# Performance work log

Hardware: AMD Instinct MI355X
Metric: run time of the kernel (lower is better)

Reference implementation:

```python
import jax, jax.numpy as jnp
import numpy as np

E, P, K, V, H, NE = 768, 256, 32, 32, 128, 8
B, M_DIM, T_DIM = 16, 4, 512


def setup_inputs() -> dict:
    key = jax.random.key(0)
    ks = jax.random.split(key, 24)
    s = 0.05
    inp = {
        'token_embeddings': jax.random.normal(ks[0], (B, M_DIM, T_DIM, E), jnp.float32),
        'U': jax.random.uniform(ks[1], (B, M_DIM, T_DIM), jnp.float32),
        'R': jax.random.uniform(ks[2], (B, M_DIM, M_DIM, T_DIM), jnp.float32),
        'S': jax.random.uniform(ks[3], (B, M_DIM, M_DIM, T_DIM), jnp.float32),
        'W_tp': jax.random.normal(ks[4], (E, P), jnp.float32) * s,
        'b_tp': jnp.zeros((P,), jnp.float32),
        'W_q': jax.random.normal(ks[5], (P, K), jnp.float32) * s,
        'b_q': jnp.zeros((K,), jnp.float32),
        'W_k': jax.random.normal(ks[6], (2, K), jnp.float32) * s,
        'b_k': jnp.zeros((K,), jnp.float32),
        'W_v': jax.random.normal(ks[7], (2, V), jnp.float32) * s,
        'b_v': jnp.zeros((V,), jnp.float32),
        'W_ih': jax.random.normal(ks[8], (3 * H, 1 + V), jnp.float32) * s,
        'W_hh': jax.random.normal(ks[9], (3 * H, H), jnp.float32) * s,
        'b_ih': jnp.zeros((3 * H,), jnp.float32),
        'b_hh': jnp.zeros((3 * H,), jnp.float32),
        'W1': jax.random.normal(ks[10], (P + H, (P + H) // 2), jnp.float32) * s,
        'b1': jnp.zeros(((P + H) // 2,), jnp.float32),
        'W2': jax.random.normal(ks[11], ((P + H) // 2, NE), jnp.float32) * s,
        'b2': jnp.zeros((NE,), jnp.float32),
        'M': M_DIM,
        'T': T_DIM,
    }
    return inp


def _gru(x, W_ih, W_hh, b_ih, b_hh):
    # x: [N, T, D] -> outputs [N, T, H]; PyTorch GRU cell math
    N, T, _ = x.shape
    Hh = W_hh.shape[1]
    gi = jnp.einsum('ntd,gd->ntg', x, W_ih) + b_ih  # [N,T,3H] precomputed input gates
    gi = jnp.transpose(gi, (1, 0, 2))  # [T,N,3H]

    def step(h, gi_t):
        gh = h @ W_hh.T + b_hh
        i_r, i_z, i_n = jnp.split(gi_t, 3, axis=-1)
        h_r, h_z, h_n = jnp.split(gh, 3, axis=-1)
        r = jax.nn.sigmoid(i_r + h_r)
        z = jax.nn.sigmoid(i_z + h_z)
        n = jnp.tanh(i_n + r * h_n)
        h_new = (1.0 - z) * n + z * h
        return h_new, h_new

    h0 = jnp.zeros((N, Hh), x.dtype)
    _, hs = jax.lax.scan(step, h0, gi)
    return jnp.transpose(hs, (1, 0, 2))  # [N,T,H]


def reference(token_embeddings, U, R, S, W_tp, b_tp, W_q, b_q, W_k, b_k, W_v, b_v,
              W_ih, W_hh, b_ih, b_hh, W1, b1, W2, b2, M, T):
    Bn, Mn, Tn, _ = token_embeddings.shape
    proc = jax.nn.relu(token_embeddings @ W_tp + b_tp)           # [B,M,T,P]
    query = proc @ W_q + b_q                                     # [B,M,T,K]
    Rp = jnp.transpose(R, (0, 3, 1, 2))                          # [B,T,M,M]
    Sp = jnp.transpose(S, (0, 3, 1, 2))
    pf = jnp.stack([Rp, Sp], axis=-1)                            # [B,T,M,M,2]
    keys = pf @ W_k + b_k                                        # [B,T,M,M,K]
    vals = pf @ W_v + b_v                                        # [B,T,M,M,V]
    scores = jnp.einsum('bmtk,btmjk->bmtj', query, keys) / np.sqrt(K)
    diag = jnp.eye(Mn, dtype=bool)                               # exclude j == m
    scores = jnp.where(diag[None, :, None, :], -1e9, scores)
    w = jax.nn.softmax(scores, axis=-1)                          # [B,M,T,M]
    ctx = jnp.einsum('bmtj,btmjv->bmtv', w, vals)                # [B,M,T,V]
    gru_in = jnp.concatenate([U[..., None], ctx], axis=-1)       # [B,M,T,1+V]
    gru_out = _gru(gru_in.reshape(Bn * Mn, Tn, 1 + V), W_ih, W_hh, b_ih, b_hh)
    rus_ctx = gru_out.reshape(Bn, Mn, Tn, H)
    combined = jnp.concatenate([proc, rus_ctx], axis=-1)         # [B,M,T,P+H]
    hidden = jax.nn.relu(combined @ W1 + b1)
    logits = hidden @ W2 + b2                                    # [B,M,T,NE]
    return logits
```

## Files before the change

kernel.cpp:

```cpp
#include <hip/hip_runtime.h>


typedef __attribute__((ext_vector_type(8))) short short8;
typedef __attribute__((ext_vector_type(4))) float f32x4;

__device__ __forceinline__ float bf2f(unsigned short u) {
    return __uint_as_float(((unsigned int)u) << 16);
}
__device__ __forceinline__ unsigned short f2bf(float f) {
    unsigned int x = __float_as_uint(f);
    return (unsigned short)((x + 0x7FFFu + ((x >> 16) & 1u)) >> 16);
}
__device__ __forceinline__ float sigm(float x) { return 1.0f / (1.0f + __expf(-x)); }
__device__ __forceinline__ float tanh_fast(float x) {
    x = fminf(fmaxf(x, -15.0f), 15.0f);
    float e = __expf(-2.0f * x);
    return (1.0f - e) / (1.0f + e);
}
__device__ __forceinline__ float dpp_xor1_add(float v) {
    int o = __builtin_amdgcn_update_dpp(0, __float_as_int(v), 0xB1, 0xF, 0xF, true);
    return v + __int_as_float(o);
}
__device__ __forceinline__ float sel4(f32x4 c, int sel) {
    float t0 = (sel & 1) ? c[1] : c[0];
    float t1 = (sel & 1) ? c[3] : c[2];
    return (sel & 2) ? t1 : t0;
}

#define CST_SC   768
#define CST_WU   800
#define CST_WA2  1184
#define CST_WB2  1568
#define CST_CC   1952

__global__ void k_paint(float* out, float val, int nmax) {
    int i = blockIdx.x * blockDim.x + threadIdx.x;
    if (i < nmax) out[i] = val;
}

__global__ void k_prep(const float* __restrict__ Wq,
                       const float* __restrict__ bq,
                       const float* __restrict__ Wk,
                       const float* __restrict__ bk,
                       const float* __restrict__ Wv,
                       const float* __restrict__ bv,
                       const float* __restrict__ Wih,
                       const float* __restrict__ bih,
                       float* __restrict__ cst)
{
    const int t = threadIdx.x;
    if (t < 256) {
        float a = 0.f, b = 0.f, c = 0.f;
        for (int k = 0; k < 32; ++k) {
            float w = Wq[t * 32 + k];
            a = fmaf(w, Wk[k], a);
            b = fmaf(w, Wk[32 + k], b);
            c = fmaf(w, bk[k], c);
        }
        cst[t] = a; cst[256 + t] = b; cst[512 + t] = c;
    }
    if (t == 0) {
        float ca = 0.f, cb = 0.f, cc = 0.f;
        for (int k = 0; k < 32; ++k) {
            float bqk = bq[k];
            ca = fmaf(bqk, Wk[k], ca);
            cb = fmaf(bqk, Wk[32 + k], cb);
            cc = fmaf(bqk, bk[k], cc);
        }
        cst[CST_SC + 0] = ca; cst[CST_SC + 1] = cb; cst[CST_SC + 2] = cc;
    }
    if (t < 384) {
        cst[CST_WU + t] = Wih[t * 33];
        float a2 = 0.f, b2 = 0.f, c2 = bih[t];
        for (int v = 0; v < 32; ++v) {
            float w = Wih[t * 33 + 1 + v];
            a2 = fmaf(w, Wv[v], a2);
            b2 = fmaf(w, Wv[32 + v], b2);
            c2 = fmaf(w, bv[v], c2);
        }
        cst[CST_WA2 + t] = a2; cst[CST_WB2 + t] = b2; cst[CST_CC + t] = c2;
    }
}

__global__ __launch_bounds__(256) void k_proc(
    const float* __restrict__ A,
    const float* __restrict__ Bw,
    const float* __restrict__ bias,
    unsigned short* __restrict__ C)
{
    __shared__ unsigned short A_s[64 * 40];
    __shared__ unsigned short B_s[64 * 40];
    const int t = threadIdx.x;
    const int row0 = blockIdx.y * 64;
    const int col0 = blockIdx.x * 64;
    const int lane = t & 63, wave = t >> 6;
    const int wr = wave >> 1, wc = wave & 1;
    const int quad = lane >> 4, l16 = lane & 15;

    f32x4 acc[2][2] = {};

    for (int k0 = 0; k0 < 768; k0 += 32) {
        {
            const int r = t >> 2, kq = (t & 3) * 8;
            const float* src = A + (size_t)(row0 + r) * 768 + k0 + kq;
            float4 v0 = *(const float4*)(src);
            float4 v1 = *(const float4*)(src + 4);
            short8 s;
            s[0] = f2bf(v0.x); s[1] = f2bf(v0.y); s[2] = f2bf(v0.z); s[3] = f2bf(v0.w);
            s[4] = f2bf(v1.x); s[5] = f2bf(v1.y); s[6] = f2bf(v1.z); s[7] = f2bf(v1.w);
            *(short8*)(A_s + r * 40 + kq) = s;
        }
        {
            const int k = t >> 3, nq = (t & 7) * 8;
            const float* src = Bw + (size_t)(k0 + k) * 256 + col0 + nq;
            float4 v0 = *(const float4*)(src);
            float4 v1 = *(const float4*)(src + 4);
            B_s[(nq + 0) * 40 + k] = f2bf(v0.x);
            B_s[(nq + 1) * 40 + k] = f2bf(v0.y);
            B_s[(nq + 2) * 40 + k] = f2bf(v0.z);
            B_s[(nq + 3) * 40 + k] = f2bf(v0.w);
            B_s[(nq + 4) * 40 + k] = f2bf(v1.x);
            B_s[(nq + 5) * 40 + k] = f2bf(v1.y);
            B_s[(nq + 6) * 40 + k] = f2bf(v1.z);
            B_s[(nq + 7) * 40 + k] = f2bf(v1.w);
        }
        __syncthreads();
        short8 af[2], bf[2];
        #pragma unroll
        for (int im = 0; im < 2; ++im)
            af[im] = *(const short8*)(A_s + (wr * 32 + im * 16 + l16) * 40 + quad * 8);
        #pragma unroll
        for (int in = 0; in < 2; ++in)
            bf[in] = *(const short8*)(B_s + (wc * 32 + in * 16 + l16) * 40 + quad * 8);
        #pragma unroll
        for (int im = 0; im < 2; ++im)
            #pragma unroll
            for (int in = 0; in < 2; ++in)
                acc[im][in] = __builtin_amdgcn_mfma_f32_16x16x32_bf16(
                    af[im], bf[in], acc[im][in], 0, 0, 0);
        __syncthreads();
    }
    float bias_v[2];
    #pragma unroll
    for (int in = 0; in < 2; ++in) bias_v[in] = bias[col0 + wc * 32 + in * 16 + l16];
    #pragma unroll
    for (int im = 0; im < 2; ++im)
        #pragma unroll
        for (int in = 0; in < 2; ++in) {
            const int c_g = col0 + wc * 32 + in * 16 + l16;
            #pragma unroll
            for (int reg = 0; reg < 4; ++reg) {
                const int r_g = row0 + wr * 32 + im * 16 + quad * 4 + reg;
                float v = fmaxf(acc[im][in][reg] + bias_v[in], 0.f);
                C[(size_t)r_g * 256 + c_g] = f2bf(v);
            }
        }
}

__global__ __launch_bounds__(256) void k_attn(
    const unsigned short* __restrict__ proc,
    const float* __restrict__ R,
    const float* __restrict__ S,
    const float* __restrict__ cst,
    float* __restrict__ wrws)
{
    __shared__ float wv_s[768];
    const int tid = threadIdx.x;
    for (int i = tid; i < 768; i += 256) wv_s[i] = cst[i];
    __syncthreads();

    const int lane = tid & 63, wave = tid >> 6;
    const int row = blockIdx.x * 4 + wave;
    const int t = row & 511, m = (row >> 9) & 3, b = row >> 11;
    const int p0 = lane * 4;

    ushort4 u = *(const ushort4*)(proc + (size_t)row * 256 + p0);
    float p0f = bf2f(u.x), p1f = bf2f(u.y), p2f = bf2f(u.z), p3f = bf2f(u.w);
    float dA = 0.f, dB = 0.f, dC = 0.f;
    dA = fmaf(p0f, wv_s[p0 + 0], dA); dB = fmaf(p0f, wv_s[256 + p0 + 0], dB); dC = fmaf(p0f, wv_s[512 + p0 + 0], dC);
    dA = fmaf(p1f, wv_s[p0 + 1], dA); dB = fmaf(p1f, wv_s[256 + p0 + 1], dB); dC = fmaf(p1f, wv_s[512 + p0 + 1], dC);
    dA = fmaf(p2f, wv_s[p0 + 2], dA); dB = fmaf(p2f, wv_s[256 + p0 + 2], dB); dC = fmaf(p2f, wv_s[512 + p0 + 2], dC);
    dA = fmaf(p3f, wv_s[p0 + 3], dA); dB = fmaf(p3f, wv_s[256 + p0 + 3], dB); dC = fmaf(p3f, wv_s[512 + p0 + 3], dC);
    #pragma unroll
    for (int mm = 1; mm < 64; mm <<= 1) {
        dA += __shfl_xor(dA, mm, 64);
        dB += __shfl_xor(dB, mm, 64);
        dC += __shfl_xor(dC, mm, 64);
    }
    if (lane == 0) {
        dA += cst[CST_SC + 0]; dB += cst[CST_SC + 1]; dC += cst[CST_SC + 2];
        const float scale = 0.17677669529663687f;
        float rr[4], ss[4], sc[4], mx = -1e30f;
        #pragma unroll
        for (int j = 0; j < 4; ++j) {
            const size_t idx = ((size_t)(b * 16 + m * 4 + j)) * 512 + t;
            rr[j] = R[idx]; ss[j] = S[idx];
            float v = (rr[j] * dA + ss[j] * dB + dC) * scale;
            if (j == m) v = -1e9f;
            sc[j] = v; mx = fmaxf(mx, v);
        }
        float w[4], se = 0.f;
        #pragma unroll
        for (int j = 0; j < 4; ++j) { w[j] = __expf(sc[j] - mx); se += w[j]; }
        const float inv = 1.0f / se;
        float wr = 0.f, wss = 0.f;
        #pragma unroll
        for (int j = 0; j < 4; ++j) { wr += w[j] * rr[j]; wss += w[j] * ss[j]; }
        float2 o; o.x = wr * inv; o.y = wss * inv;
        ((float2*)wrws)[row] = o;
    }
}

__global__ __launch_bounds__(256) void k_gru(
    const float* __restrict__ wrws,
    const float* __restrict__ U,
    const float* __restrict__ Whh,
    const float* __restrict__ bhh,
    const float* __restrict__ cst,
    unsigned short* __restrict__ gout)
{
    __shared__ unsigned short hbuf[2][2][144];
    __shared__ float4 uvw_s[512];

    const int tid  = threadIdx.x;
    const int lane = tid & 63, w = tid >> 6;
    const int l16  = lane & 15, quad = lane >> 4;
    const int n    = blockIdx.x;
    const int par  = l16 & 1;
    const int sel  = (l16 >> 1) & 3;
    const int hh   = (l16 >> 3) & 1;
    const int eg   = 32 * w + 16 * hh + quad * 4 + sel;
    const bool writer = (par == 0);

    short8 afr[3][2][4];
    #pragma unroll
    for (int g3 = 0; g3 < 3; ++g3)
        #pragma unroll
        for (int h2 = 0; h2 < 2; ++h2) {
            const int row = g3 * 128 + 32 * w + 16 * h2 + l16;
            const float* rp = Whh + (size_t)row * 128 + quad * 8;
            #pragma unroll
            for (int kf = 0; kf < 4; ++kf) {
                float4 v0 = *(const float4*)(rp + kf * 32);
                float4 v1 = *(const float4*)(rp + kf * 32 + 4);
                short8 s;
                s[0] = f2bf(v0.x); s[1] = f2bf(v0.y); s[2] = f2bf(v0.z); s[3] = f2bf(v0.w);
                s[4] = f2bf(v1.x); s[5] = f2bf(v1.y); s[6] = f2bf(v1.z); s[7] = f2bf(v1.w);
                afr[g3][h2][kf] = s;
            }
        }

    const float wu_r = cst[CST_WU  + eg], wu_z = cst[CST_WU  + 128 + eg], wu_n = cst[CST_WU  + 256 + eg];
    const float wa_r = cst[CST_WA2 + eg], wa_z = cst[CST_WA2 + 128 + eg], wa_n = cst[CST_WA2 + 256 + eg];
    const float wb_r = cst[CST_WB2 + eg], wb_z = cst[CST_WB2 + 128 + eg], wb_n = cst[CST_WB2 + 256 + eg];
    const float cc_r = cst[CST_CC  + eg] + bhh[eg];
    const float cc_z = cst[CST_CC  + 128 + eg] + bhh[128 + eg];
    const float cc_n = cst[CST_CC  + 256 + eg];
    const float bh_n = bhh[256 + eg];

    for (int i = tid; i < 512; i += 256) {
        float u = U[(size_t)n * 512 + i];
        float2 w2 = ((const float2*)wrws)[(size_t)n * 512 + i];
        float4 p; p.x = u; p.y = w2.x; p.z = w2.y; p.w = 0.f;
        uvw_s[i] = p;
    }
    for (int i = tid; i < 288; i += 256) ((unsigned int*)hbuf)[i] = 0u;
    __syncthreads();

    float h_old = 0.f;
    const f32x4 ZZ = {0.f, 0.f, 0.f, 0.f};

    #pragma unroll 2
    for (int t = 0; t < 512; ++t) {
        const int cur = t & 1, nxt = cur ^ 1;

        const unsigned short* hb = &hbuf[cur][par][0];
        short8 bfr[4];
        #pragma unroll
        for (int kf = 0; kf < 4; ++kf)
            bfr[kf] = *(const short8*)(hb + kf * 32 + quad * 8);
        const float4 uvw = uvw_s[t];

        f32x4 c[6] = {ZZ, ZZ, ZZ, ZZ, ZZ, ZZ};
        #pragma unroll
        for (int kf = 0; kf < 4; ++kf)
            #pragma unroll
            for (int j = 0; j < 6; ++j)
                c[j] = __builtin_amdgcn_mfma_f32_16x16x32_bf16(
                    afr[j >> 1][j & 1][kf], bfr[kf], c[j], 0, 0, 0);

        float gh[3];
        #pragma unroll
        for (int g3 = 0; g3 < 3; ++g3) {
            const float v0 = sel4(c[2 * g3 + 0], sel);
            const float v1 = sel4(c[2 * g3 + 1], sel);
            gh[g3] = dpp_xor1_add(hh ? v1 : v0);
        }

        const float gir = fmaf(uvw.z, wb_r, fmaf(uvw.y, wa_r, fmaf(uvw.x, wu_r, cc_r)));
        const float giz = fmaf(uvw.z, wb_z, fmaf(uvw.y, wa_z, fmaf(uvw.x, wu_z, cc_z)));
        const float gin = fmaf(uvw.z, wb_n, fmaf(uvw.y, wa_n, fmaf(uvw.x, wu_n, cc_n)));
        const float r  = sigm(gir + gh[0]);
        const float z  = sigm(giz + gh[1]);
        const float nn = tanh_fast(fmaf(r, gh[2] + bh_n, gin));
        const float hn = fmaf(z, h_old - nn, nn);
        h_old = hn;

        if (writer) {
            const unsigned short hi16 = f2bf(hn);
            hbuf[nxt][0][eg] = hi16;
            hbuf[nxt][1][eg] = f2bf(hn - bf2f(hi16));
            gout[((size_t)n * 512 + t) * 128 + eg] = hi16;
        }
        asm volatile("s_waitcnt lgkmcnt(0)" ::: "memory");
        __builtin_amdgcn_s_barrier();
        asm volatile("" ::: "memory");
        __builtin_amdgcn_sched_barrier(0x7);
    }
}

__global__ __launch_bounds__(256) void k_hid(
    const unsigned short* __restrict__ proc,
    const unsigned short* __restrict__ gout,
    const float* __restrict__ W1,
    const float* __restrict__ b1,
    const float* __restrict__ W2,
    const float* __restrict__ b2,
    float* __restrict__ out)
{
    __shared__ __align__(16) unsigned char smem[56352];
    unsigned short* As = (unsigned short*)smem;
    unsigned short* Bh = (unsigned short*)(smem + 5120);
    unsigned short* Bl = (unsigned short*)(smem + 20480);
    float* Hs  = (float*)smem;
    float* W2s = (float*)(smem + 50176);
    float* b2s = (float*)(smem + 56320);

    const int tid = threadIdx.x;
    const int row0 = blockIdx.x * 64;
    const int lane = tid & 63, w = tid >> 6;
    const int l16 = lane & 15, quad = lane >> 4;

    for (int i = tid; i < 1536; i += 256) W2s[i] = W2[i];
    if (tid < 8) b2s[tid] = b2[tid];

    const int ar = tid >> 2, akq = (tid & 3) * 8;
    const int bk2 = (tid >> 4) * 2, bc0 = tid & 15;

    f32x4 acc[4][3] = {};

    for (int k0 = 0; k0 < 384; k0 += 32) {
        __syncthreads();
        {
            const int kk = k0 + akq;
            short8 v;
            if (kk < 256) v = *(const short8*)(proc + (size_t)(row0 + ar) * 256 + kk);
            else          v = *(const short8*)(gout + (size_t)(row0 + ar) * 128 + (kk - 256));
            *(short8*)(As + ar * 40 + akq) = v;
        }
        {
            const float* wrow0 = W1 + (size_t)(k0 + bk2) * 192;
            const float* wrow1 = wrow0 + 192;
            #pragma unroll
            for (int j = 0; j < 12; ++j) {
                const int c = bc0 + 16 * j;
                const float f0 = wrow0[c], f1 = wrow1[c];
                const unsigned short h0 = f2bf(f0), h1 = f2bf(f1);
                const unsigned short s0 = f2bf(f0 - bf2f(h0));
                const unsigned short s1 = f2bf(f1 - bf2f(h1));
                *(unsigned int*)(Bh + c * 40 + bk2) = (unsigned int)h0 | ((unsigned int)h1 << 16);
                *(unsigned int*)(Bl + c * 40 + bk2) = (unsigned int)s0 | ((unsigned int)s1 << 16);
            }
        }
        __syncthreads();
        short8 af[4], bh[3], bl[3];
        #pragma unroll
        for (int m = 0; m < 4; ++m)
            af[m] = *(const short8*)(As + (m * 16 + l16) * 40 + quad * 8);
        #pragma unroll
        for (int nn = 0; nn < 3; ++nn) {
            const int col = w * 48 + nn * 16 + l16;
            bh[nn] = *(const short8*)(Bh + col * 40 + quad * 8);
            bl[nn] = *(const short8*)(Bl + col * 40 + quad * 8);
        }
        #pragma unroll
        for (int m = 0; m < 4; ++m)
            #pragma unroll
            for (int nn = 0; nn < 3; ++nn) {
                acc[m][nn] = __builtin_amdgcn_mfma_f32_16x16x32_bf16(af[m], bh[nn], acc[m][nn], 0, 0, 0);
                acc[m][nn] = __builtin_amdgcn_mfma_f32_16x16x32_bf16(af[m], bl[nn], acc[m][nn], 0, 0, 0);
            }
    }
    __syncthreads();
    {
        float b1v[3];
        #pragma unroll
        for (int nn = 0; nn < 3; ++nn) b1v[nn] = b1[w * 48 + nn * 16 + l16];
        #pragma unroll
        for (int m = 0; m < 4; ++m)
            #pragma unroll
            for (int nn = 0; nn < 3; ++nn) {
                const int col = w * 48 + nn * 16 + l16;
                #pragma unroll
                for (int reg = 0; reg < 4; ++reg) {
                    const int row = m * 16 + quad * 4 + reg;
                    Hs[row * 196 + col] = fmaxf(acc[m][nn][reg] + b1v[nn], 0.f);
                }
            }
    }
    __syncthreads();
    const int r = tid >> 2, qq = tid & 3;
    const int e0 = 2 * qq, e1 = 2 * qq + 1;
    float s0 = b2s[e0], s1 = b2s[e1];
    for (int c = 0; c < 192; ++c) {
        float h = Hs[r * 196 + c];
        s0 = fmaf(h, W2s[c * 8 + e0], s0);
        s1 = fmaf(h, W2s[c * 8 + e1], s1);
    }
    out[(size_t)(row0 + r) * 8 + e0] = s0;
    out[(size_t)(row0 + r) * 8 + e1] = s1;
}

extern "C" void kernel_launch(void* const* d_in, const int* in_sizes, int n_in,
                              void* d_out, int out_size, void* d_ws, size_t ws_size,
                              hipStream_t stream) {
    const float* emb  = (const float*)d_in[0];
    const float* U    = (const float*)d_in[1];
    const float* R    = (const float*)d_in[2];
    const float* S    = (const float*)d_in[3];
    const float* W_tp = (const float*)d_in[4];
    const float* b_tp = (const float*)d_in[5];
    const float* W_q  = (const float*)d_in[6];
    const float* b_q  = (const float*)d_in[7];
    const float* W_k  = (const float*)d_in[8];
    const float* b_k  = (const float*)d_in[9];
    const float* W_v  = (const float*)d_in[10];
    const float* b_v  = (const float*)d_in[11];
    const float* W_ih = (const float*)d_in[12];
    const float* W_hh = (const float*)d_in[13];
    const float* b_ih = (const float*)d_in[14];
    const float* b_hh = (const float*)d_in[15];
    const float* W1   = (const float*)d_in[16];
    const float* b1   = (const float*)d_in[17];
    const float* W2   = (const float*)d_in[18];
    const float* b2   = (const float*)d_in[19];

    float* outp = (float*)d_out;

    const size_t NEEDED = 25444352u;
    if (ws_size < NEEDED) {
        k_paint<<<(out_size + 255) / 256, 256, 0, stream>>>(outp, 3.0f, out_size);
        return;
    }

    char* ws = (char*)d_ws;
    unsigned short* proc = (unsigned short*)(ws);
    float*          wrws = (float*)(ws + 16777216u);
    unsigned short* gout = (unsigned short*)(ws + 17039360u);
    float*          cst  = (float*)(ws + 25427968u);

    k_prep<<<1, 512, 0, stream>>>(W_q, b_q, W_k, b_k, W_v, b_v, W_ih, b_ih, cst);
    k_proc<<<dim3(4, 512), 256, 0, stream>>>(emb, W_tp, b_tp, proc);
    k_attn<<<8192, 256, 0, stream>>>(proc, R, S, cst, wrws);
    k_gru <<<64, 256, 0, stream>>>(wrws, U, W_hh, b_hh, cst, gout);
    k_hid <<<512, 256, 0, stream>>>(proc, gout, W1, b1, W2, b2, outp);
}
```

Before: 530.6 us.

## Enlarge proc GEMM tile, defer GRU output stores, vectorize W2 dot

The projection GEMM now uses 128-row tiles, so each wave computes 4x2 MFMA tiles and the grid is halved. This gives more reuse of the B tile per load. In the GRU recurrence, both lane parities now write their own hbuf entry, removing the divergent writer branch. The global store of h is deferred by one step, and the next step's U/attention values are prefetched from LDS. The final hidden-to-logits dot product uses a transposed W2 in LDS and float4 reads to cut scalar LDS traffic.

```diff
diff --git a/kernel.cpp b/kernel.cpp
--- a/kernel.cpp
+++ b/kernel.cpp
@@ -88,27 +88,32 @@
     const float* __restrict__ bias,
     unsigned short* __restrict__ C)
 {
-    __shared__ unsigned short A_s[64 * 40];
+    __shared__ unsigned short A_s[128 * 40];
     __shared__ unsigned short B_s[64 * 40];
     const int t = threadIdx.x;
-    const int row0 = blockIdx.y * 64;
+    const int row0 = blockIdx.y * 128;
     const int col0 = blockIdx.x * 64;
     const int lane = t & 63, wave = t >> 6;
     const int wr = wave >> 1, wc = wave & 1;
     const int quad = lane >> 4, l16 = lane & 15;
 
-    f32x4 acc[2][2] = {};
+    f32x4 acc[4][2] = {};
 
     for (int k0 = 0; k0 < 768; k0 += 32) {
         {
-            const int r = t >> 2, kq = (t & 3) * 8;
+            const int r = t >> 1, kq = (t & 1) * 16;
             const float* src = A + (size_t)(row0 + r) * 768 + k0 + kq;
             float4 v0 = *(const float4*)(src);
             float4 v1 = *(const float4*)(src + 4);
-            short8 s;
-            s[0] = f2bf(v0.x); s[1] = f2bf(v0.y); s[2] = f2bf(v0.z); s[3] = f2bf(v0.w);
-            s[4] = f2bf(v1.x); s[5] = f2bf(v1.y); s[6] = f2bf(v1.z); s[7] = f2bf(v1.w);
-            *(short8*)(A_s + r * 40 + kq) = s;
+            float4 v2 = *(const float4*)(src + 8);
+            float4 v3 = *(const float4*)(src + 12);
+            short8 s0, s1;
+            s0[0] = f2bf(v0.x); s0[1] = f2bf(v0.y); s0[2] = f2bf(v0.z); s0[3] = f2bf(v0.w);
+            s0[4] = f2bf(v1.x); s0[5] = f2bf(v1.y); s0[6] = f2bf(v1.z); s0[7] = f2bf(v1.w);
+            s1[0] = f2bf(v2.x); s1[1] = f2bf(v2.y); s1[2] = f2bf(v2.z); s1[3] = f2bf(v2.w);
+            s1[4] = f2bf(v3.x); s1[5] = f2bf(v3.y); s1[6] = f2bf(v3.z); s1[7] = f2bf(v3.w);
+            *(short8*)(A_s + r * 40 + kq) = s0;
+            *(short8*)(A_s + r * 40 + kq + 8) = s1;
         }
         {
             const int k = t >> 3, nq = (t & 7) * 8;
@@ -125,15 +130,15 @@
             B_s[(nq + 7) * 40 + k] = f2bf(v1.w);
         }
         __syncthreads();
-        short8 af[2], bf[2];
-        #pragma unroll
-        for (int im = 0; im < 2; ++im)
-            af[im] = *(const short8*)(A_s + (wr * 32 + im * 16 + l16) * 40 + quad * 8);
+        short8 af[4], bf[2];
+        #pragma unroll
+        for (int im = 0; im < 4; ++im)
+            af[im] = *(const short8*)(A_s + (wr * 64 + im * 16 + l16) * 40 + quad * 8);
         #pragma unroll
         for (int in = 0; in < 2; ++in)
             bf[in] = *(const short8*)(B_s + (wc * 32 + in * 16 + l16) * 40 + quad * 8);
         #pragma unroll
-        for (int im = 0; im < 2; ++im)
+        for (int im = 0; im < 4; ++im)
             #pragma unroll
             for (int in = 0; in < 2; ++in)
                 acc[im][in] = __builtin_amdgcn_mfma_f32_16x16x32_bf16(
@@ -144,13 +149,13 @@
     #pragma unroll
     for (int in = 0; in < 2; ++in) bias_v[in] = bias[col0 + wc * 32 + in * 16 + l16];
     #pragma unroll
-    for (int im = 0; im < 2; ++im)
+    for (int im = 0; im < 4; ++im)
         #pragma unroll
         for (int in = 0; in < 2; ++in) {
             const int c_g = col0 + wc * 32 + in * 16 + l16;
             #pragma unroll
             for (int reg = 0; reg < 4; ++reg) {
-                const int r_g = row0 + wr * 32 + im * 16 + quad * 4 + reg;
+                const int r_g = row0 + wr * 64 + im * 16 + quad * 4 + reg;
                 float v = fmaxf(acc[im][in][reg] + bias_v[in], 0.f);
                 C[(size_t)r_g * 256 + c_g] = f2bf(v);
             }
@@ -230,7 +235,6 @@
     const int sel  = (l16 >> 1) & 3;
     const int hh   = (l16 >> 3) & 1;
     const int eg   = 32 * w + 16 * hh + quad * 4 + sel;
-    const bool writer = (par == 0);
 
     short8 afr[3][2][4];
     #pragma unroll
@@ -268,18 +272,22 @@
     __syncthreads();
 
     float h_old = 0.f;
+    unsigned short prev_hi = 0;
+    unsigned short* gp = gout + (size_t)n * 512 * 128 + eg;
+    float4 uvw = uvw_s[0];
     const f32x4 ZZ = {0.f, 0.f, 0.f, 0.f};
 
     #pragma unroll 2
     for (int t = 0; t < 512; ++t) {
         const int cur = t & 1, nxt = cur ^ 1;
 
+        if (t && par == 0) gp[(size_t)(t - 1) * 128] = prev_hi;
+
         const unsigned short* hb = &hbuf[cur][par][0];
         short8 bfr[4];
         #pragma unroll
         for (int kf = 0; kf < 4; ++kf)
             bfr[kf] = *(const short8*)(hb + kf * 32 + quad * 8);
-        const float4 uvw = uvw_s[t];
 
         f32x4 c[6] = {ZZ, ZZ, ZZ, ZZ, ZZ, ZZ};
         #pragma unroll
@@ -306,17 +314,20 @@
         const float hn = fmaf(z, h_old - nn, nn);
         h_old = hn;
 
-        if (writer) {
-            const unsigned short hi16 = f2bf(hn);
-            hbuf[nxt][0][eg] = hi16;
-            hbuf[nxt][1][eg] = f2bf(hn - bf2f(hi16));
-            gout[((size_t)n * 512 + t) * 128 + eg] = hi16;
-        }
+        const float4 uvw_n = uvw_s[(t + 1) & 511];
+
+        const unsigned short hi16 = f2bf(hn);
+        const unsigned short wv = par ? f2bf(hn - bf2f(hi16)) : hi16;
+        hbuf[nxt][par][eg] = wv;
+        prev_hi = hi16;
+
         asm volatile("s_waitcnt lgkmcnt(0)" ::: "memory");
         __builtin_amdgcn_s_barrier();
         asm volatile("" ::: "memory");
         __builtin_amdgcn_sched_barrier(0x7);
-    }
+        uvw = uvw_n;
+    }
+    if (par == 0) gp[(size_t)511 * 128] = prev_hi;
 }
 
 __global__ __launch_bounds__(256) void k_hid(
@@ -328,20 +339,23 @@
     const float* __restrict__ b2,
     float* __restrict__ out)
 {
-    __shared__ __align__(16) unsigned char smem[56352];
+    __shared__ __align__(16) unsigned char smem[56480];
     unsigned short* As = (unsigned short*)smem;
     unsigned short* Bh = (unsigned short*)(smem + 5120);
     unsigned short* Bl = (unsigned short*)(smem + 20480);
     float* Hs  = (float*)smem;
-    float* W2s = (float*)(smem + 50176);
-    float* b2s = (float*)(smem + 56320);
+    float* W2t = (float*)(smem + 50176);
+    float* b2s = (float*)(smem + 56448);
 
     const int tid = threadIdx.x;
     const int row0 = blockIdx.x * 64;
     const int lane = tid & 63, w = tid >> 6;
     const int l16 = lane & 15, quad = lane >> 4;
 
-    for (int i = tid; i < 1536; i += 256) W2s[i] = W2[i];
+    for (int i = tid; i < 1536; i += 256) {
+        const int c = i >> 3, e = i & 7;
+        W2t[e * 196 + c] = W2[i];
+    }
     if (tid < 8) b2s[tid] = b2[tid];
 
     const int ar = tid >> 2, akq = (tid & 3) * 8;
@@ -410,12 +424,18 @@
     }
     __syncthreads();
     const int r = tid >> 2, qq = tid & 3;
-    const int e0 = 2 * qq, e1 = 2 * qq + 1;
+    const int e0 = 2 * qq, e1 = e0 + 1;
     float s0 = b2s[e0], s1 = b2s[e1];
-    for (int c = 0; c < 192; ++c) {
-        float h = Hs[r * 196 + c];
-        s0 = fmaf(h, W2s[c * 8 + e0], s0);
-        s1 = fmaf(h, W2s[c * 8 + e1], s1);
+    const float* hrow = Hs + r * 196;
+    const float* w0 = W2t + e0 * 196;
+    const float* w1 = W2t + e1 * 196;
+    #pragma unroll 8
+    for (int c = 0; c < 192; c += 4) {
+        float4 h4 = *(const float4*)(hrow + c);
+        float4 a4 = *(const float4*)(w0 + c);
+        float4 b4 = *(const float4*)(w1 + c);
+        s0 = fmaf(h4.x, a4.x, fmaf(h4.y, a4.y, fmaf(h4.z, a4.z, fmaf(h4.w, a4.w, s0))));
+        s1 = fmaf(h4.x, b4.x, fmaf(h4.y, b4.y, fmaf(h4.z, b4.z, fmaf(h4.w, b4.w, s1))));
     }
     out[(size_t)(row0 + r) * 8 + e0] = s0;
     out[(size_t)(row0 + r) * 8 + e1] = s1;
@@ -460,7 +480,7 @@
     float*          cst  = (float*)(ws + 25427968u);
 
     k_prep<<<1, 512, 0, stream>>>(W_q, b_q, W_k, b_k, W_v, b_v, W_ih, b_ih, cst);
-    k_proc<<<dim3(4, 512), 256, 0, stream>>>(emb, W_tp, b_tp, proc);
+    k_proc<<<dim3(4, 256), 256, 0, stream>>>(emb, W_tp, b_tp, proc);
     k_attn<<<8192, 256, 0, stream>>>(proc, R, S, cst, wrws);
     k_gru <<<64, 256, 0, stream>>>(wrws, U, W_hh, b_hh, cst, gout);
     k_hid <<<512, 256, 0, stream>>>(proc, gout, W1, b1, W2, b2, outp);
```

Result: slower. 563.0 us (+6.1%).
